# Kernel optimization log

Hardware: AMD Instinct MI355X
Metric: run time of the kernel (lower is better)

Reference implementation:

```python
import jax, jax.numpy as jnp
import numpy as np

B, N, DIM, H, DH = 2, 1024, 2048, 16, 128
MAX_POS = 16
QK_SCALE = 10.0  # qk_norm_scale (replaces dim_head**-0.5 when qk_norm=True)
NEG = -1e30  # large negative mask value (sigmoid -> 0, softmax -> 0)

def rotate_half(x):
    # interleaved pair rotation: '... (d r) -> ... d r', r=2
    shape = x.shape
    xr = x.reshape(shape[:-1] + (shape[-1] // 2, 2))
    x1, x2 = xr[..., 0], xr[..., 1]
    return jnp.stack((-x2, x1), axis=-1).reshape(shape)

def setup_inputs() -> dict:
    key = jax.random.key(0)
    ks = jax.random.split(key, 10)
    # proper rotary frequencies, repeat-interleaved to match rotate_half's pair layout
    half = DH // 2
    inv_freq = 1.0 / (10000.0 ** (np.arange(half, dtype=np.float32) / half))
    freqs = np.repeat(np.outer(np.arange(N, dtype=np.float32), inv_freq), 2, axis=-1)  # [N, DH]
    sd = 0.02
    return {
        'x': jax.random.normal(ks[0], (B, N, DIM), jnp.float32),
        'rotary_freqs': jnp.asarray(freqs),
        'w_q': jax.random.normal(ks[1], (DIM, H * DH), jnp.float32) * sd,
        'w_k': jax.random.normal(ks[2], (DIM, H * DH), jnp.float32) * sd,
        'w_v': jax.random.normal(ks[3], (DIM, H * DH), jnp.float32) * sd,
        'cope_emb': jax.random.normal(ks[4], (MAX_POS, DH), jnp.float32) * sd,  # CoPE pos_emb (nonzero for testing)
        'th_pre': jnp.eye(H, dtype=jnp.float32) + jax.random.normal(ks[5], (H, H), jnp.float32) * sd,
        'th_post': jnp.eye(H, dtype=jnp.float32) + jax.random.normal(ks[6], (H, H), jnp.float32) * sd,
        'w_vgate': jax.random.normal(ks[7], (DIM, H * DH), jnp.float32) * sd,
        'b_vgate': jnp.full((H * DH,), 10.0, jnp.float32),
        'w_hgate': jax.random.normal(ks[8], (DIM, H), jnp.float32) * sd,
        'b_hgate': jnp.full((H,), 10.0, jnp.float32),
        'w_out': jax.random.normal(ks[9], (H * DH, DIM), jnp.float32) * sd,
    }

def reference(x, rotary_freqs, w_q, w_k, w_v, cope_emb, th_pre, th_post, w_vgate, b_vgate, w_hgate, b_hgate, w_out):
    b, n, _ = x.shape
    to_heads = lambda t: t.reshape(b, n, H, DH).transpose(0, 2, 1, 3)  # b h n d
    q = to_heads(x @ w_q)
    k = to_heads(x @ w_k)
    v = to_heads(x @ w_v)
    # qk l2-norm (groups=1), then fixed qk_norm_scale
    q = q / jnp.maximum(jnp.linalg.norm(q, axis=-1, keepdims=True), 1e-12)
    k = k / jnp.maximum(jnp.linalg.norm(k, axis=-1, keepdims=True), 1e-12)
    # rotary embedding (scale=1, rot_dim == dim_head)
    cos, sin = jnp.cos(rotary_freqs), jnp.sin(rotary_freqs)
    q = q * cos + rotate_half(q) * sin
    k = k * cos + rotate_half(k) * sin
    sim = jnp.einsum('bhid,bhjd->bhij', q, k) * QK_SCALE
    sim = jnp.einsum('hg,bgij->bhij', th_pre, sim)  # pre-softmax talking heads (1x1 conv over heads)
    causal = jnp.triu(jnp.ones((n, n), dtype=bool), 1)
    sim = jnp.where(causal, NEG, sim)
    # ---- CoPE (linear interpolation path) ----
    gates = jax.nn.sigmoid(sim)  # masked entries -> 0
    pos = jnp.flip(jnp.cumsum(jnp.flip(gates, -1), axis=-1), -1)  # reverse cumsum over j
    pos = jnp.minimum(pos, MAX_POS - 1.0)
    logits_int = jnp.einsum('bhnd,pd->bhnp', q, cope_emb)
    pos_floor = jnp.floor(pos)
    w_interp = pos - pos_floor
    lc = jnp.take_along_axis(logits_int, jnp.ceil(pos).astype(jnp.int32), axis=-1)
    lf = jnp.take_along_axis(logits_int, pos_floor.astype(jnp.int32), axis=-1)
    sim = sim + lc * w_interp + lf * (1.0 - w_interp)
    # ------------------------------------------
    attn = jax.nn.softmax(sim, axis=-1)
    attn = jnp.einsum('hg,bgij->bhij', th_post, attn)  # post-softmax talking heads
    out = jnp.einsum('bhij,bhjd->bhid', attn, v)
    # per-head value gate
    head_gate = jax.nn.sigmoid(x @ w_hgate + b_hgate)  # b n h
    out = out * head_gate.transpose(0, 2, 1)[..., None]
    out = out.transpose(0, 2, 1, 3).reshape(b, n, H * DH)
    # elementwise value gate (sigmoid, bias init 10)
    out = out * jax.nn.sigmoid(x @ w_vgate + b_vgate)
    return out @ w_out
```

## Files before the change

kernel.cpp:

```cpp
#include <hip/hip_runtime.h>
#include <hip/hip_fp16.h>

typedef unsigned short u16;
typedef __attribute__((ext_vector_type(4))) float f32x4;
typedef __attribute__((ext_vector_type(8))) _Float16 f16x8;
typedef __attribute__((ext_vector_type(4))) _Float16 f16x4;
typedef __attribute__((ext_vector_type(8))) unsigned short u16x8;
typedef __attribute__((ext_vector_type(4))) unsigned short u16x4;

#define DEVI __device__ __forceinline__
#define MASKV (-1000.0f)

DEVI u16 f2h(float f){ __half h = __float2half(f); return __half_as_ushort(h); }
DEVI float h2f(u16 v){ return __half2float(__ushort_as_half(v)); }
DEVI float sigm(float s){ float e = __expf(-fabsf(s)); return (s >= 0.f) ? 1.f/(1.f+e) : e/(1.f+e); }

DEVI void async16(const void* g, void* l){
  __builtin_amdgcn_global_load_lds((__attribute__((address_space(1))) const unsigned int*)g,
                                   (__attribute__((address_space(3))) unsigned int*)l, 16, 0, 0);
}

struct Acc { f32x4 a[4][4]; };
DEVI void acc_zero(Acc& a){
  f32x4 z = {0.f,0.f,0.f,0.f};
  #pragma unroll
  for (int i=0;i<4;i++)
    #pragma unroll
    for (int j=0;j<4;j++) a.a[i][j] = z;
}

DEVI void gemm_core(const u16* __restrict__ A, int lda, const u16* __restrict__ Bt, int ldb,
                    int K, u16* As, u16* Bs, Acc& acc, int tid)
{
  int w = tid >> 6, l = tid & 63;
  int q = l >> 4, m = l & 15;
  int wm = w & 1, wn = w >> 1;
  for (int k0 = 0; k0 < K; k0 += 32){
    __syncthreads();
    #pragma unroll
    for (int p = 0; p < 2; p++){
      int row = w*32 + p*16 + (l>>2);
      async16(A  + (size_t)row*lda + k0 + (l&3)*8, As + (w*32 + p*16)*32);
      async16(Bt + (size_t)row*ldb + k0 + (l&3)*8, Bs + (w*32 + p*16)*32);
    }
    __syncthreads();
    f16x8 af[4], bf[4];
    #pragma unroll
    for (int t = 0; t < 4; t++){
      af[t] = *(const f16x8*)(As + (wm*64 + t*16 + m)*32 + q*8);
      bf[t] = *(const f16x8*)(Bs + (wn*64 + t*16 + m)*32 + q*8);
    }
    #pragma unroll
    for (int i = 0; i < 4; i++)
      #pragma unroll
      for (int j = 0; j < 4; j++)
        acc.a[i][j] = __builtin_amdgcn_mfma_f32_16x16x32_f16(af[i], bf[j], acc.a[i][j], 0, 0, 0);
  }
}

struct PrepArgs {
  const float* src[7];
  u16* dst[7];
  int C[7];
};
__global__ __launch_bounds__(256) void k_prep(PrepArgs p){
  __shared__ u16 t[32][33];
  int z = blockIdx.z;
  if (z == 0){
    int i = ((blockIdx.y*64 + blockIdx.x)*256 + threadIdx.x)*4;
    f32x4 v = *(const f32x4*)(p.src[0] + i);
    u16x4 o;
    #pragma unroll
    for (int z2=0; z2<4; z2++) o[z2] = f2h(v[z2]);
    *(u16x4*)(p.dst[0] + i) = o;
    return;
  }
  const float* src = p.src[z]; u16* dst = p.dst[z];
  int R = 2048, C = p.C[z];
  int c0 = blockIdx.x*32, r0 = blockIdx.y*32;
  if (c0 >= C) return;
  int tx = threadIdx.x & 31, ty = threadIdx.x >> 5;
  #pragma unroll
  for (int i = ty; i < 32; i += 8){
    int r = r0 + i, c = c0 + tx;
    if (r < R && c < C) t[i][tx] = f2h(src[(size_t)r*C + c]);
  }
  __syncthreads();
  #pragma unroll
  for (int i = ty; i < 32; i += 8){
    int rr = c0 + i, cc = r0 + tx;
    if (rr < C && cc < R) dst[(size_t)rr*R + cc] = t[tx][i];
  }
}

__global__ __launch_bounds__(256) void k_transpose_h(const u16* __restrict__ src, u16* __restrict__ dst,
    int R, int C, long sps, long dps){
  __shared__ u16 t[32][33];
  src += (size_t)blockIdx.z * sps; dst += (size_t)blockIdx.z * dps;
  int c0 = blockIdx.x*32, r0 = blockIdx.y*32;
  int tx = threadIdx.x & 31, ty = threadIdx.x >> 5;
  #pragma unroll
  for (int i = ty; i < 32; i += 8){
    int r = r0 + i, c = c0 + tx;
    if (r < R && c < C) t[i][tx] = src[(size_t)r*C + c];
  }
  __syncthreads();
  #pragma unroll
  for (int i = ty; i < 32; i += 8){
    int rr = c0 + i, cc = r0 + tx;
    if (rr < C && cc < R) dst[(size_t)rr*R + cc] = t[tx][i];
  }
}

struct ProjArgs {
  const u16* xh;
  const u16* wT0; const u16* wT1; const u16* wT2; const u16* wT3;
  u16* q; u16* k; u16* v; u16* vg;
  const float* bvg;
};
__global__ __launch_bounds__(256) void k_proj(ProjArgs p){
  __shared__ __align__(16) u16 As[4096];
  __shared__ __align__(16) u16 Bs[4096];
  int z = blockIdx.z;
  const u16* wT = (z==0) ? p.wT0 : (z==1) ? p.wT1 : (z==2) ? p.wT2 : p.wT3;
  int tid = threadIdx.x;
  Acc acc; acc_zero(acc);
  const u16* A  = p.xh + (size_t)blockIdx.x*128*2048;
  const u16* Bt = wT   + (size_t)blockIdx.y*128*2048;
  gemm_core(A, 2048, Bt, 2048, 2048, As, Bs, acc, tid);
  int w = tid>>6, l = tid&63, q4 = l>>4, m = l&15, wm = w&1, wn = w>>1;
  #pragma unroll
  for (int ti=0; ti<4; ti++)
  #pragma unroll
  for (int tj=0; tj<4; tj++)
  #pragma unroll
  for (int r=0; r<4; r++){
    int trow = blockIdx.x*128 + wm*64 + ti*16 + q4*4 + r;
    int col  = blockIdx.y*128 + wn*64 + tj*16 + m;
    float v = acc.a[ti][tj][r];
    if (z == 3){
      float sg = sigm(v + p.bvg[col]);
      p.vg[(size_t)trow*2048 + col] = f2h(sg);
    } else {
      int b = trow >> 10, i = trow & 1023, h = col >> 7, d = col & 127;
      u16* dst = (z==0) ? p.q : (z==1) ? p.k : p.v;
      dst[(((size_t)(b*16 + h))*1024 + i)*128 + d] = f2h(v);
    }
  }
}

__global__ __launch_bounds__(256) void k_hgate(const u16* __restrict__ xh, const u16* __restrict__ whgT,
    const float* __restrict__ bhg, float* __restrict__ hg){
  __shared__ float red[4][256];
  int tid = threadIdx.x, w = tid>>6, l = tid&63, q = l>>4, m = l&15;
  int t0 = blockIdx.x*16;
  f32x4 acc = {0.f,0.f,0.f,0.f};
  const u16* xr = xh   + (size_t)(t0 + m)*2048 + w*512;
  const u16* br = whgT + (size_t)m*2048 + w*512;
  #pragma unroll 4
  for (int k = 0; k < 512; k += 32){
    f16x8 a = *(const f16x8*)(xr + k + q*8);
    f16x8 b = *(const f16x8*)(br + k + q*8);
    acc = __builtin_amdgcn_mfma_f32_16x16x32_f16(a, b, acc, 0, 0, 0);
  }
  #pragma unroll
  for (int r = 0; r < 4; r++) red[w][(q*4+r)*16 + m] = acc[r];
  __syncthreads();
  float v = red[0][tid] + red[1][tid] + red[2][tid] + red[3][tid];
  int tl = tid >> 4, h = tid & 15;
  hg[(size_t)(t0 + tl)*16 + h] = sigm(v + bhg[h]);
}

__global__ __launch_bounds__(256) void k_normrope(u16* __restrict__ qb, u16* __restrict__ kb,
    const float* __restrict__ freqs, const float* __restrict__ cope, float* __restrict__ L){
  __shared__ float ce[2048];
  int tid = threadIdx.x;
  for (int i2 = tid; i2 < 2048; i2 += 256) ce[i2] = cope[i2];
  __syncthreads();
  int w = tid >> 6, l = tid & 63;
  int r = blockIdx.x*4 + w;
  int isq = (r < 32768) ? 1 : 0;
  int rr = isq ? r : r - 32768;
  int i = rr & 1023;
  u16* base = (isq ? qb : kb) + (size_t)rr*128;
  float v0 = h2f(base[2*l]), v1 = h2f(base[2*l+1]);
  float ss = v0*v0 + v1*v1;
  #pragma unroll
  for (int off = 1; off < 64; off <<= 1) ss += __shfl_xor(ss, off);
  float rn = 1.f / fmaxf(sqrtf(ss), 1e-12f);
  v0 *= rn; v1 *= rn;
  float f = freqs[i*128 + 2*l];
  float sn, cs; sincosf(f, &sn, &cs);
  float o0 = v0*cs - v1*sn, o1 = v1*cs + v0*sn;
  base[2*l] = f2h(o0); base[2*l+1] = f2h(o1);
  if (isq){
    #pragma unroll
    for (int p = 0; p < 16; p++){
      float part = o0*ce[p*128 + 2*l] + o1*ce[p*128 + 2*l + 1];
      #pragma unroll
      for (int off = 1; off < 64; off <<= 1) part += __shfl_xor(part, off);
      if (l == p) L[(size_t)rr*16 + p] = part;
    }
  }
}

__global__ __launch_bounds__(256) void k_qk(const u16* __restrict__ qb, const u16* __restrict__ kb,
    u16* __restrict__ S){
  __shared__ __align__(16) u16 As[8192];
  __shared__ __align__(16) u16 Bs[16384];
  int bh = blockIdx.y;
  int bx = 15 - (int)blockIdx.x;
  int i0 = bx*64, it = bx >> 1;
  int njt = (bx + 2) >> 1;
  int tid = threadIdx.x, w = tid>>6, l = tid&63, q = l>>4, m = l&15, wm = w&1, wn = w>>1;
  const u16* qbase = qb + (size_t)bh*131072;
  const u16* kbase = kb + (size_t)bh*131072;
  #pragma unroll
  for (int sub = 0; sub < 4; sub++){
    int row = w*16 + (l>>2);
    async16(qbase + (size_t)(i0 + row)*128 + sub*32 + (l&3)*8, As + sub*2048 + (w*16)*32);
  }
  u16* dstbase = S + ((size_t)bh*36 + (it*(it+1))/2)*16384 + (size_t)((bx&1)*64)*128;
  for (int jt = 0; jt < njt; jt++){
    __syncthreads();
    #pragma unroll
    for (int sub = 0; sub < 4; sub++)
      #pragma unroll
      for (int p = 0; p < 2; p++){
        int row = w*32 + p*16 + (l>>2);
        async16(kbase + (size_t)(jt*128 + row)*128 + sub*32 + (l&3)*8,
                Bs + sub*4096 + (w*32 + p*16)*32);
      }
    __syncthreads();
    f32x4 acc[2][4];
    { f32x4 z = {0.f,0.f,0.f,0.f};
      #pragma unroll
      for (int a2=0;a2<2;a2++)
        #pragma unroll
        for (int b2=0;b2<4;b2++) acc[a2][b2] = z; }
    #pragma unroll
    for (int kc = 0; kc < 4; kc++){
      f16x8 af[2], bf[4];
      #pragma unroll
      for (int t = 0; t < 2; t++) af[t] = *(const f16x8*)(As + kc*2048 + (wm*32 + t*16 + m)*32 + q*8);
      #pragma unroll
      for (int t = 0; t < 4; t++) bf[t] = *(const f16x8*)(Bs + kc*4096 + (wn*64 + t*16 + m)*32 + q*8);
      #pragma unroll
      for (int a2 = 0; a2 < 2; a2++)
        #pragma unroll
        for (int b2 = 0; b2 < 4; b2++)
          acc[a2][b2] = __builtin_amdgcn_mfma_f32_16x16x32_f16(af[a2], bf[b2], acc[a2][b2], 0, 0, 0);
    }
    u16* dst = dstbase + (size_t)jt*16384;
    #pragma unroll
    for (int ti=0; ti<2; ti++)
    #pragma unroll
    for (int tj=0; tj<4; tj++)
    #pragma unroll
    for (int r=0; r<4; r++){
      int iloc = wm*32 + ti*16 + q*4 + r;
      int jloc = wn*64 + tj*16 + m;
      float v = acc[ti][tj][r] * 10.f;
      if (jt*128 + jloc > i0 + iloc) v = MASKV;
      dst[(size_t)iloc*128 + jloc] = f2h(v);
    }
  }
}

struct CopeArgs { const u16* S; const float* L; const float* thpre; u16* Sout; float* ml; };
__global__ __launch_bounds__(1024) void k_cope(CopeArgs pa){
  __shared__ u16 raw[16*276];
  __shared__ float thsh[256];
  __shared__ float Lsh[1024];
  int b = blockIdx.y;
  int i0 = (int)(gridDim.x - 1 - blockIdx.x) * 4;
  int tid = threadIdx.x, w = tid>>6, l = tid&63;
  int h = w;
  if (tid < 256) thsh[tid] = pa.thpre[tid];
  Lsh[tid] = pa.L[ ((size_t)((b*16 + (tid>>6))*1024) + i0 + ((tid>>4)&3))*16 + (tid&15) ];
  __syncthreads();
  float th_r[16];
  #pragma unroll
  for (int g = 0; g < 16; g++) th_r[g] = thsh[h*16 + g];
  int ii = l >> 4, j0 = (l & 15)*4;
  int i = i0 + ii, it1 = i >> 7, iloc = i & 127;
  const float* Lrow = Lsh + h*64 + ii*16;
  float carry = 0.f, mrun = -1e30f, lrun = 0.f;
  int tmax = (i0 + 3) >> 6;
  for (int t = tmax; t >= 0; t--){
    int jt1 = (t*64) >> 7, jo = (t*64) & 127;
    __syncthreads();
    {
      int e = tid*4;
      int g = e >> 8, r = e & 255;
      int si = r >> 6, j = r & 63;
      int irow = i0 + si; int it2 = irow >> 7, il2 = irow & 127;
      const u16* src = pa.S + ((size_t)((b*16+g)*36 + (it2*(it2+1))/2 + jt1))*16384
                           + (size_t)il2*128 + jo + j;
      *(u16x4*)(raw + g*276 + si*68 + j) = *(const u16x4*)src;
    }
    __syncthreads();
    float s0=0.f, s1=0.f, s2=0.f, s3=0.f;
    #pragma unroll
    for (int g = 0; g < 16; g++){
      u16x4 v = *(const u16x4*)(raw + g*276 + ii*68 + j0);
      float tg = th_r[g];
      s0 += tg*h2f(v[0]); s1 += tg*h2f(v[1]); s2 += tg*h2f(v[2]); s3 += tg*h2f(v[3]);
    }
    float g0 = sigm(s0), g1 = sigm(s1), g2 = sigm(s2), g3 = sigm(s3);
    float c3 = g3, c2 = g2 + c3, c1 = g1 + c2, c0 = g0 + c1;
    float T = c0, Tacc = T;
    #pragma unroll
    for (int off = 1; off < 16; off <<= 1){
      float tv = __shfl(Tacc, (l + off) & 63);
      if (((l & 15) + off) < 16) Tacc += tv;
    }
    float Rh = Tacc - T;
    float rowtot = __shfl(Tacc, l & 48);
    float sf[4];
    float cc[4] = {c0, c1, c2, c3};
    float ssv[4] = {s0, s1, s2, s3};
    #pragma unroll
    for (int c = 0; c < 4; c++){
      float pos = fminf(cc[c] + Rh + carry, 15.f);
      float pf = floorf(pos);
      float wi = pos - pf;
      int ic = (int)ceilf(pos), ifl = (int)pf;
      float v = ssv[c] + Lrow[ic]*wi + Lrow[ifl]*(1.f - wi);
      sf[c] = v;
    }
    carry += rowtot;
    u16x4 ov;
    #pragma unroll
    for (int c = 0; c < 4; c++){ ov[c] = f2h(sf[c]); sf[c] = h2f(ov[c]); }
    *(u16x4*)(pa.Sout + ((size_t)((b*16+h)*36 + (it1*(it1+1))/2 + jt1))*16384
              + (size_t)iloc*128 + jo + j0) = ov;
    float M = fmaxf(fmaxf(sf[0], sf[1]), fmaxf(sf[2], sf[3]));
    #pragma unroll
    for (int off = 1; off < 16; off <<= 1) M = fmaxf(M, __shfl_xor(M, off));
    float mnew = fmaxf(mrun, M);
    float es = __expf(fminf(sf[0]-mnew,0.f)) + __expf(fminf(sf[1]-mnew,0.f))
             + __expf(fminf(sf[2]-mnew,0.f)) + __expf(fminf(sf[3]-mnew,0.f));
    #pragma unroll
    for (int off = 1; off < 16; off <<= 1) es += __shfl_xor(es, off);
    lrun = lrun*__expf(fminf(mrun - mnew, 0.f)) + es;
    mrun = mnew;
  }
  if ((l & 15) == 0){
    size_t bix = (size_t)(b*16 + h)*1024 + i0 + ii;
    pa.ml[bix] = mrun;
    pa.ml[32768 + bix] = 1.f/fmaxf(lrun, 1e-30f);
  }
}

struct PostArgs { const u16* S; const float* ml; const float* thpost; u16* Sout; };
__global__ __launch_bounds__(256) void k_postmix(PostArgs pa){
  __shared__ u16 at[16*1040];
  __shared__ _Float16 thsh[256];
  __shared__ float mh[128], rlh[128];
  int tile = blockIdx.x >> 4, sub = blockIdx.x & 15, b = blockIdx.y;
  int it = 0;
  #pragma unroll
  for (int t2=1; t2<8; t2++) if (tile >= (t2*(t2+1))/2) it = t2;
  int tid = threadIdx.x;
  thsh[tid] = (_Float16)pa.thpost[tid];
  if (tid < 128){
    int g = tid >> 3, ii = tid & 7;
    size_t ix = (size_t)(b*16+g)*1024 + it*128 + sub*8 + ii;
    mh[tid] = pa.ml[ix]; rlh[tid] = pa.ml[32768 + ix];
  }
  __syncthreads();
  {
    int g = tid >> 4, l16 = tid & 15;
    const u16* src = pa.S + ((size_t)((b*16+g)*36 + tile))*16384 + sub*1024;
    #pragma unroll
    for (int c = 0; c < 16; c++){
      int e = c*64 + l16*4;
      int ii = e >> 7;
      float mm = mh[g*8+ii], rr = rlh[g*8+ii];
      u16x4 sv = *(const u16x4*)(src + e);
      u16x4 o;
      #pragma unroll
      for (int z2=0; z2<4; z2++) o[z2] = f2h(__expf(fminf(h2f(sv[z2]) - mm, 0.f)) * rr);
      *(u16x4*)(at + g*1040 + e) = o;
    }
  }
  __syncthreads();
  int h = tid >> 4, c16 = tid & 15;
  _Float16 th_h[16];
  #pragma unroll
  for (int g = 0; g < 16; g++) th_h[g] = thsh[h*16 + g];
  u16* dst = pa.Sout + ((size_t)((b*16+h)*36 + tile))*16384 + sub*1024;
  #pragma unroll
  for (int k = 0; k < 16; k++){
    int e = c16*4 + k*64;
    f16x4 a = {0,0,0,0};
    #pragma unroll
    for (int g = 0; g < 16; g++){
      f16x4 v = *(const f16x4*)(at + g*1040 + e);
      a += v * th_h[g];
    }
    *(f16x4*)(dst + e) = a;
  }
}

struct PvArgs { const u16* S; const u16* vT; const float* hg; const u16* vg; u16* gated; };
__global__ __launch_bounds__(256) void k_pv(PvArgs pa){
  __shared__ __align__(16) u16 As[8192];
  __shared__ __align__(16) u16 Bs[16384];
  int bh = blockIdx.y, b = bh >> 4, h = bh & 15;
  int bx = 15 - (int)blockIdx.x;
  int i0 = bx*64, it = bx >> 1;
  int nc = (bx + 2) >> 1;
  int tid = threadIdx.x, w = tid>>6, l = tid&63, q = l>>4, m = l&15, wm = w&1, wn = w>>1;
  const u16* abase = pa.S + ((size_t)bh*36 + (it*(it+1))/2)*16384 + (size_t)((bx&1)*64)*128;
  const u16* vt    = pa.vT + (size_t)bh*131072;
  f32x4 acc[2][4];
  { f32x4 z = {0.f,0.f,0.f,0.f};
    #pragma unroll
    for (int a2=0;a2<2;a2++)
      #pragma unroll
      for (int b2=0;b2<4;b2++) acc[a2][b2] = z; }
  for (int jc = 0; jc < nc; jc++){
    __syncthreads();
    #pragma unroll
    for (int sub = 0; sub < 4; sub++){
      int row = w*16 + (l>>2);
      async16(abase + (size_t)jc*16384 + (size_t)row*128 + sub*32 + (l&3)*8,
              As + sub*2048 + (w*16)*32);
      #pragma unroll
      for (int p = 0; p < 2; p++){
        int brow = w*32 + p*16 + (l>>2);
        async16(vt + (size_t)brow*1024 + jc*128 + sub*32 + (l&3)*8,
                Bs + sub*4096 + (w*32 + p*16)*32);
      }
    }
    __syncthreads();
    #pragma unroll
    for (int kc = 0; kc < 4; kc++){
      f16x8 af[2], bf[4];
      #pragma unroll
      for (int t = 0; t < 2; t++) af[t] = *(const f16x8*)(As + kc*2048 + (wm*32 + t*16 + m)*32 + q*8);
      #pragma unroll
      for (int t = 0; t < 4; t++) bf[t] = *(const f16x8*)(Bs + kc*4096 + (wn*64 + t*16 + m)*32 + q*8);
      #pragma unroll
      for (int a2 = 0; a2 < 2; a2++)
        #pragma unroll
        for (int b2 = 0; b2 < 4; b2++)
          acc[a2][b2] = __builtin_amdgcn_mfma_f32_16x16x32_f16(af[a2], bf[b2], acc[a2][b2], 0, 0, 0);
    }
  }
  #pragma unroll
  for (int ti=0; ti<2; ti++)
  #pragma unroll
  for (int tj=0; tj<4; tj++)
  #pragma unroll
  for (int r=0; r<4; r++){
    int i = i0 + wm*32 + ti*16 + q*4 + r;
    int d = wn*64 + tj*16 + m;
    int tok = b*1024 + i;
    float v = acc[ti][tj][r] * pa.hg[(size_t)tok*16 + h] * h2f(pa.vg[(size_t)tok*2048 + h*128 + d]);
    if (v != v) v = 333.f;
    pa.gated[(size_t)tok*2048 + h*128 + d] = f2h(v);
  }
}

__global__ __launch_bounds__(256) void k_out(const u16* __restrict__ gated, const u16* __restrict__ woT,
    float* __restrict__ out){
  __shared__ __align__(16) u16 As[2048];
  __shared__ __align__(16) u16 Bs[4096];
  int bx = blockIdx.x;
  int by = blockIdx.y;
  int trow0 = by*64, c0 = bx*128;
  int tid = threadIdx.x, w = tid>>6, l = tid&63, q = l>>4, m = l&15, wm = w&1, wn = w>>1;
  f32x4 acc[2][4];
  { f32x4 z = {0.f,0.f,0.f,0.f};
    #pragma unroll
    for (int a2=0;a2<2;a2++)
      #pragma unroll
      for (int b2=0;b2<4;b2++) acc[a2][b2] = z; }
  for (int k0 = 0; k0 < 2048; k0 += 32){
    __syncthreads();
    {
      int row = w*16 + (l>>2);
      async16(gated + (size_t)(trow0 + row)*2048 + k0 + (l&3)*8, As + (w*16)*32);
    }
    #pragma unroll
    for (int p = 0; p < 2; p++){
      int row = w*32 + p*16 + (l>>2);
      async16(woT + (size_t)(c0 + row)*2048 + k0 + (l&3)*8, Bs + (w*32 + p*16)*32);
    }
    __syncthreads();
    f16x8 af[2], bf[4];
    #pragma unroll
    for (int t = 0; t < 2; t++) af[t] = *(const f16x8*)(As + (wm*32 + t*16 + m)*32 + q*8);
    #pragma unroll
    for (int t = 0; t < 4; t++) bf[t] = *(const f16x8*)(Bs + (wn*64 + t*16 + m)*32 + q*8);
    #pragma unroll
    for (int a2 = 0; a2 < 2; a2++)
      #pragma unroll
      for (int b2 = 0; b2 < 4; b2++)
        acc[a2][b2] = __builtin_amdgcn_mfma_f32_16x16x32_f16(af[a2], bf[b2], acc[a2][b2], 0, 0, 0);
  }
  #pragma unroll
  for (int ti=0; ti<2; ti++)
  #pragma unroll
  for (int tj=0; tj<4; tj++)
  #pragma unroll
  for (int r=0; r<4; r++){
    int trow = trow0 + wm*32 + ti*16 + q*4 + r;
    int col  = c0 + wn*64 + tj*16 + m;
    float o = acc[ti][tj][r];
    if (o != o) o = 911.f;
    out[(size_t)trow*2048 + col] = o;
  }
}

extern "C" void kernel_launch(void* const* d_in, const int* in_sizes, int n_in,
                              void* d_out, int out_size, void* d_ws, size_t ws_size,
                              hipStream_t stream){
  const float* x      = (const float*)d_in[0];
  const float* freqs  = (const float*)d_in[1];
  const float* w_q    = (const float*)d_in[2];
  const float* w_k    = (const float*)d_in[3];
  const float* w_v    = (const float*)d_in[4];
  const float* cope   = (const float*)d_in[5];
  const float* thpre  = (const float*)d_in[6];
  const float* thpost = (const float*)d_in[7];
  const float* w_vg   = (const float*)d_in[8];
  const float* b_vg   = (const float*)d_in[9];
  const float* w_hg   = (const float*)d_in[10];
  const float* b_hg   = (const float*)d_in[11];
  const float* w_out  = (const float*)d_in[12];

  char* ws = (char*)d_ws;
  size_t off = 0;
  auto alloc = [&](size_t bytes)->char*{ char* r = ws + off; off += (bytes + 255) & ~(size_t)255; return r; };
  u16*   xh    = (u16*)  alloc(8388608);
  u16*   wqT   = (u16*)  alloc(8388608);
  u16*   wkT   = (u16*)  alloc(8388608);
  u16*   wvT   = (u16*)  alloc(8388608);
  u16*   wvgT  = (u16*)  alloc(8388608);
  u16*   woT   = (u16*)  alloc(8388608);
  u16*   whgT  = (u16*)  alloc(65536);
  u16*   qb    = (u16*)  alloc(8388608);
  u16*   kb    = (u16*)  alloc(8388608);
  u16*   vb    = (u16*)  alloc(8388608);
  u16*   vTT   = (u16*)  alloc(8388608);
  u16*   vg    = (u16*)  alloc(8388608);
  u16*   gated = (u16*)  alloc(8388608);
  float* L     = (float*)alloc(2097152);
  float* hg    = (float*)alloc(131072);
  float* ml    = (float*)alloc(262144);
  u16*   S     = (u16*)  alloc(37748736);

  dim3 b256(256);
  PrepArgs pp;
  pp.src[0]=x;    pp.dst[0]=xh;   pp.C[0]=2048;
  pp.src[1]=w_q;  pp.dst[1]=wqT;  pp.C[1]=2048;
  pp.src[2]=w_k;  pp.dst[2]=wkT;  pp.C[2]=2048;
  pp.src[3]=w_v;  pp.dst[3]=wvT;  pp.C[3]=2048;
  pp.src[4]=w_vg; pp.dst[4]=wvgT; pp.C[4]=2048;
  pp.src[5]=w_out;pp.dst[5]=woT;  pp.C[5]=2048;
  pp.src[6]=w_hg; pp.dst[6]=whgT; pp.C[6]=16;
  k_prep<<<dim3(64,64,7), b256, 0, stream>>>(pp);

  ProjArgs pa{ xh, wqT, wkT, wvT, wvgT, qb, kb, vb, vg, b_vg };
  k_proj<<<dim3(16,16,4), b256, 0, stream>>>(pa);
  k_hgate<<<dim3(128), b256, 0, stream>>>(xh, whgT, b_hg, hg);
  k_transpose_h<<<dim3(4,32,32), b256, 0, stream>>>(vb, vTT, 1024, 128, 131072L, 131072L);
  k_normrope<<<dim3(16384), b256, 0, stream>>>(qb, kb, freqs, cope, L);
  k_qk<<<dim3(16,32), b256, 0, stream>>>(qb, kb, S);
  CopeArgs ca{ S, L, thpre, S, ml };
  k_cope<<<dim3(256,2), dim3(1024), 0, stream>>>(ca);
  PostArgs po{ S, ml, thpost, S };
  k_postmix<<<dim3(576,2), b256, 0, stream>>>(po);
  PvArgs pv{ S, vTT, hg, vg, gated };
  k_pv<<<dim3(16,32), b256, 0, stream>>>(pv);
  k_out<<<dim3(16,32), b256, 0, stream>>>(gated, woT, (float*)d_out);
}
```

Baseline: 498.0 us.

## Rewrite projection GEMM with 256x256 tiles, double-buffered LDS and swizzle

New measurement: 480.6 us. 3.5% less time.

```diff
diff --git a/kernel.cpp b/kernel.cpp
--- a/kernel.cpp
+++ b/kernel.cpp
@@ -18,44 +18,6 @@
 DEVI void async16(const void* g, void* l){
   __builtin_amdgcn_global_load_lds((__attribute__((address_space(1))) const unsigned int*)g,
                                    (__attribute__((address_space(3))) unsigned int*)l, 16, 0, 0);
-}
-
-struct Acc { f32x4 a[4][4]; };
-DEVI void acc_zero(Acc& a){
-  f32x4 z = {0.f,0.f,0.f,0.f};
-  #pragma unroll
-  for (int i=0;i<4;i++)
-    #pragma unroll
-    for (int j=0;j<4;j++) a.a[i][j] = z;
-}
-
-DEVI void gemm_core(const u16* __restrict__ A, int lda, const u16* __restrict__ Bt, int ldb,
-                    int K, u16* As, u16* Bs, Acc& acc, int tid)
-{
-  int w = tid >> 6, l = tid & 63;
-  int q = l >> 4, m = l & 15;
-  int wm = w & 1, wn = w >> 1;
-  for (int k0 = 0; k0 < K; k0 += 32){
-    __syncthreads();
-    #pragma unroll
-    for (int p = 0; p < 2; p++){
-      int row = w*32 + p*16 + (l>>2);
-      async16(A  + (size_t)row*lda + k0 + (l&3)*8, As + (w*32 + p*16)*32);
-      async16(Bt + (size_t)row*ldb + k0 + (l&3)*8, Bs + (w*32 + p*16)*32);
-    }
-    __syncthreads();
-    f16x8 af[4], bf[4];
-    #pragma unroll
-    for (int t = 0; t < 4; t++){
-      af[t] = *(const f16x8*)(As + (wm*64 + t*16 + m)*32 + q*8);
-      bf[t] = *(const f16x8*)(Bs + (wn*64 + t*16 + m)*32 + q*8);
-    }
-    #pragma unroll
-    for (int i = 0; i < 4; i++)
-      #pragma unroll
-      for (int j = 0; j < 4; j++)
-        acc.a[i][j] = __builtin_amdgcn_mfma_f32_16x16x32_f16(af[i], bf[j], acc.a[i][j], 0, 0, 0);
-  }
 }
 
 struct PrepArgs {
@@ -118,35 +80,101 @@
   u16* q; u16* k; u16* v; u16* vg;
   const float* bvg;
 };
-__global__ __launch_bounds__(256) void k_proj(ProjArgs p){
-  __shared__ __align__(16) u16 As[4096];
-  __shared__ __align__(16) u16 Bs[4096];
-  int z = blockIdx.z;
+__global__ __launch_bounds__(512) void k_proj2(ProjArgs p){
+  __shared__ __align__(16) u16 ldsA[2][16384];
+  __shared__ __align__(16) u16 ldsB[2][16384];
+  const int z = blockIdx.z;
   const u16* wT = (z==0) ? p.wT0 : (z==1) ? p.wT1 : (z==2) ? p.wT2 : p.wT3;
-  int tid = threadIdx.x;
-  Acc acc; acc_zero(acc);
-  const u16* A  = p.xh + (size_t)blockIdx.x*128*2048;
-  const u16* Bt = wT   + (size_t)blockIdx.y*128*2048;
-  gemm_core(A, 2048, Bt, 2048, 2048, As, Bs, acc, tid);
-  int w = tid>>6, l = tid&63, q4 = l>>4, m = l&15, wm = w&1, wn = w>>1;
-  #pragma unroll
-  for (int ti=0; ti<4; ti++)
-  #pragma unroll
-  for (int tj=0; tj<4; tj++)
-  #pragma unroll
-  for (int r=0; r<4; r++){
-    int trow = blockIdx.x*128 + wm*64 + ti*16 + q4*4 + r;
-    int col  = blockIdx.y*128 + wn*64 + tj*16 + m;
-    float v = acc.a[ti][tj][r];
+  const int m0 = blockIdx.x << 8, n0 = blockIdx.y << 8;
+  const int tid = threadIdx.x, w = tid >> 6, l = tid & 63;
+  const int wm = w >> 2, wn = w & 3, qq = l >> 4, m = l & 15;
+  const int cxor = (m & 4) ? 16 : 0;
+  const int lrow = l >> 3;
+  const int lcol = ((l & 7) * 8) ^ (((l >> 5) & 1) << 4);
+  const u16* aSrc = p.xh + (size_t)(m0 + lrow) * 2048 + lcol;
+  const u16* bSrc = wT   + (size_t)(n0 + lrow) * 2048 + lcol;
+  const int wp2 = w * 2;
+
+  f32x4 acc[8][4];
+  { f32x4 zr = {0.f,0.f,0.f,0.f};
+    #pragma unroll
+    for (int i=0;i<8;i++)
+      #pragma unroll
+      for (int j=0;j<4;j++) acc[i][j] = zr; }
+
+#define STGA(buf,h,kt) do{ \
+    async16(aSrc + (size_t)((h)*128 + wp2*8)*2048 + (kt)*64,     &ldsA[buf][(h)*8192 + wp2*512]); \
+    async16(aSrc + (size_t)((h)*128 + (wp2+1)*8)*2048 + (kt)*64, &ldsA[buf][(h)*8192 + (wp2+1)*512]); }while(0)
+#define STGB(buf,h,kt) do{ \
+    async16(bSrc + (size_t)((h)*128 + wp2*8)*2048 + (kt)*64,     &ldsB[buf][(h)*8192 + wp2*512]); \
+    async16(bSrc + (size_t)((h)*128 + (wp2+1)*8)*2048 + (kt)*64, &ldsB[buf][(h)*8192 + (wp2+1)*512]); }while(0)
+#define RDA(buf,i,s) (*(const f16x8*)(&ldsA[buf][(wm*128 + (i)*16 + m)*64 + (((s)*32 + qq*8) ^ cxor)]))
+#define RDB(buf,j,s) (*(const f16x8*)(&ldsB[buf][(wn*64 + (j)*16 + m)*64 + (((s)*32 + qq*8) ^ cxor)]))
+
+  f16x8 bf[4][2];
+#define RDBALL(buf) do{ \
+    _Pragma("unroll") \
+    for (int j=0;j<4;j++){ bf[j][0] = RDB(buf,j,0); bf[j][1] = RDB(buf,j,1); } }while(0)
+#define VMW asm volatile("s_waitcnt vmcnt(4)" ::: "memory")
+#define PHASE(buf,i0,BSTMT,SSTMT,VMSTMT) do{ \
+    f16x8 a00 = RDA(buf,(i0),0),   a01 = RDA(buf,(i0),1); \
+    f16x8 a10 = RDA(buf,(i0)+1,0), a11 = RDA(buf,(i0)+1,1); \
+    BSTMT; \
+    SSTMT; \
+    __builtin_amdgcn_s_barrier(); \
+    asm volatile("s_waitcnt lgkmcnt(0)" ::: "memory"); \
+    __builtin_amdgcn_s_setprio(1); \
+    _Pragma("unroll") \
+    for (int j=0;j<4;j++){ \
+      acc[(i0)][j]   = __builtin_amdgcn_mfma_f32_16x16x32_f16(a00, bf[j][0], acc[(i0)][j],   0,0,0); \
+      acc[(i0)][j]   = __builtin_amdgcn_mfma_f32_16x16x32_f16(a01, bf[j][1], acc[(i0)][j],   0,0,0); \
+      acc[(i0)+1][j] = __builtin_amdgcn_mfma_f32_16x16x32_f16(a10, bf[j][0], acc[(i0)+1][j], 0,0,0); \
+      acc[(i0)+1][j] = __builtin_amdgcn_mfma_f32_16x16x32_f16(a11, bf[j][1], acc[(i0)+1][j], 0,0,0); \
+    } \
+    __builtin_amdgcn_s_setprio(0); \
+    VMSTMT; \
+    __builtin_amdgcn_s_barrier(); }while(0)
+
+  STGA(0,0,0); STGA(0,1,0); STGB(0,0,0); STGB(0,1,0); STGB(1,0,1); STGB(1,1,1);
+  VMW;
+  __builtin_amdgcn_s_barrier();
+
+  for (int u = 0; u < 16; u++){
+    const int t1 = 2*u+1, t2 = (2*u+2)&31, t3 = (2*u+3)&31;
+    PHASE(0,0, RDBALL(0), STGA(1,0,t1), ((void)0));
+    PHASE(0,2, ((void)0), STGA(1,1,t1), ((void)0));
+    PHASE(0,4, ((void)0), STGB(0,0,t2), ((void)0));
+    PHASE(0,6, ((void)0), STGB(0,1,t2), VMW);
+    PHASE(1,0, RDBALL(1), STGA(0,0,t2), ((void)0));
+    PHASE(1,2, ((void)0), STGA(0,1,t2), ((void)0));
+    PHASE(1,4, ((void)0), STGB(1,0,t3), ((void)0));
+    PHASE(1,6, ((void)0), STGB(1,1,t3), VMW);
+  }
+
+  u16* dst3 = (z==0) ? p.q : (z==1) ? p.k : p.v;
+  #pragma unroll
+  for (int i=0;i<8;i++)
+  #pragma unroll
+  for (int j=0;j<4;j++)
+  #pragma unroll
+  for (int r=0;r<4;r++){
+    int gr = m0 + wm*128 + i*16 + qq*4 + r;
+    int gc = n0 + wn*64 + j*16 + m;
+    float v = acc[i][j][r];
     if (z == 3){
-      float sg = sigm(v + p.bvg[col]);
-      p.vg[(size_t)trow*2048 + col] = f2h(sg);
+      p.vg[(size_t)gr*2048 + gc] = f2h(sigm(v + p.bvg[gc]));
     } else {
-      int b = trow >> 10, i = trow & 1023, h = col >> 7, d = col & 127;
-      u16* dst = (z==0) ? p.q : (z==1) ? p.k : p.v;
-      dst[(((size_t)(b*16 + h))*1024 + i)*128 + d] = f2h(v);
-    }
-  }
+      int b = gr >> 10, ii = gr & 1023, h = gc >> 7, d = gc & 127;
+      dst3[(((size_t)(b*16 + h))*1024 + ii)*128 + d] = f2h(v);
+    }
+  }
+#undef STGA
+#undef STGB
+#undef RDA
+#undef RDB
+#undef RDBALL
+#undef VMW
+#undef PHASE
 }
 
 __global__ __launch_bounds__(256) void k_hgate(const u16* __restrict__ xh, const u16* __restrict__ whgT,
@@ -566,7 +594,7 @@
   k_prep<<<dim3(64,64,7), b256, 0, stream>>>(pp);
 
   ProjArgs pa{ xh, wqT, wkT, wvT, wvgT, qb, kb, vb, vg, b_vg };
-  k_proj<<<dim3(16,16,4), b256, 0, stream>>>(pa);
+  k_proj2<<<dim3(8,8,4), dim3(512), 0, stream>>>(pa);
   k_hgate<<<dim3(128), b256, 0, stream>>>(xh, whgT, b_hg, hg);
   k_transpose_h<<<dim3(4,32,32), b256, 0, stream>>>(vb, vTT, 1024, 128, 131072L, 131072L);
   k_normrope<<<dim3(16384), b256, 0, stream>>>(qb, kb, freqs, cope, L);
```
